# Optimization experiments

Hardware: AMD Instinct MI355X
Metric: run time of the kernel (lower is better)

Reference implementation:

```python
import jax, jax.numpy as jnp
import numpy as np

E = 64          # num experts
IN = 512        # input_size
OUT = 512       # output_size
N = 131072      # total tokens = sum(expert_size)
CAP = 3072      # static per-expert capacity (>= max expert_size)


def _make_expert_sizes():
    # uneven but deterministic sizes summing to N, all <= CAP
    rng = np.random.default_rng(0)
    sizes = np.full(E, N // E, dtype=np.int32)
    d = rng.integers(0, 513, size=E // 2).astype(np.int32)
    sizes[0::2] += d
    sizes[1::2] -= d
    assert sizes.sum() == N and sizes.max() <= CAP and sizes.min() > 0
    return jnp.asarray(sizes, dtype=jnp.int32)


def setup_inputs() -> dict:
    key = jax.random.key(0)
    k1, k2 = jax.random.split(key)
    inputs = jax.random.normal(k1, (N, IN), dtype=jnp.float32)
    # matches nn.init.uniform_(weight, -1/in, 1/in)
    weight = jax.random.uniform(k2, (E, IN, OUT), dtype=jnp.float32,
                                minval=-1.0 / IN, maxval=1.0 / IN)
    expert_size = _make_expert_sizes()
    return {"inputs": inputs, "expert_size": expert_size, "weight": weight}


def reference(inputs, expert_size, weight):
    # Grouped GEMM: tokens are pre-sorted by expert; segment e is
    # inputs[offset[e]:offset[e]+expert_size[e]] @ weight[e].
    cap_ids = jnp.arange(CAP, dtype=jnp.int32)                # [CAP]
    offsets = jnp.cumsum(expert_size) - expert_size           # [E]
    idx = offsets[:, None] + cap_ids[None, :]                 # [E, CAP]
    valid = cap_ids[None, :] < expert_size[:, None]           # [E, CAP]
    idx = jnp.where(valid, idx, N)                            # invalid -> OOB (dropped)
    # gather tokens into padded per-expert blocks; invalid slots -> 0
    x = jnp.take(inputs, idx, axis=0, mode='fill', fill_value=0.0)  # [E, CAP, IN]
    h = jnp.einsum('eci,eio->eco', x, weight)                 # [E, CAP, OUT]
    out = jnp.zeros((N, OUT), dtype=inputs.dtype)
    out = out.at[idx.reshape(-1)].add(h.reshape(-1, OUT), mode='drop')
    return out
```

## Files before the change

### kernel.cpp

```cpp
#include <hip/hip_runtime.h>
#include <hip/hip_bf16.h>

#define E_NUM 64
#define IN_SZ 512
#define OUT_SZ 512
#define N_TOK 131072
#define CAP 3072

#define BM 128
#define BN 256
#define BK 32
#define THREADS 256
#define RT_MAX 24
#define CT_NUM 2
#define JT 16

typedef __attribute__((ext_vector_type(8))) short short8;
typedef __attribute__((ext_vector_type(4))) float f32x4;

__device__ inline unsigned short f2bf(float f) {
    unsigned int u = __float_as_uint(f);
    unsigned int r = (u + 0x7FFF + ((u >> 16) & 1)) >> 16;
    return (unsigned short)r;
}

#define GLOAD_LDS16(g, l)                                                     \
    __builtin_amdgcn_global_load_lds(                                         \
        (const __attribute__((address_space(1))) void*)(g),                   \
        (__attribute__((address_space(3))) void*)(l), 16, 0, 0)

__global__ void offsets_kernel(const int* __restrict__ sizes, int* __restrict__ offs) {
    int e = threadIdx.x;
    int s = 0;
    for (int i = 0; i < e; ++i) s += sizes[i];
    offs[e] = s;
}

__global__ __launch_bounds__(256) void prep_wt(const float* __restrict__ W,
                                               unsigned short* __restrict__ WT) {
    __shared__ float t[32][33];
    int k0 = blockIdx.x * 32, n0 = blockIdx.y * 32, e = blockIdx.z;
    const float* We = W + (size_t)e * IN_SZ * OUT_SZ;
    int tid = threadIdx.x;
    int r = tid >> 3, c4 = (tid & 7) * 4;
    float4 v = *(const float4*)(We + (size_t)(k0 + r) * OUT_SZ + n0 + c4);
    t[r][c4 + 0] = v.x; t[r][c4 + 1] = v.y; t[r][c4 + 2] = v.z; t[r][c4 + 3] = v.w;
    __syncthreads();
    ushort4 o;
    o.x = f2bf(t[c4 + 0][r]);
    o.y = f2bf(t[c4 + 1][r]);
    o.z = f2bf(t[c4 + 2][r]);
    o.w = f2bf(t[c4 + 3][r]);
    unsigned short* O = WT + (size_t)e * IN_SZ * OUT_SZ + (size_t)(n0 + r) * IN_SZ + k0 + c4;
    *(ushort4*)O = o;
}

__global__ __launch_bounds__(THREADS, 2) void gemm_moe(
    const float* __restrict__ A, const int* __restrict__ sizes,
    const unsigned short* __restrict__ WT, const int* __restrict__ offs,
    float* __restrict__ out)
{
    int b0 = blockIdx.x;
    int wg = (b0 & 7) * (E_NUM * RT_MAX * CT_NUM / 8) + (b0 >> 3);
    int ct = wg & (CT_NUM - 1);
    int rt = (wg >> 1) % RT_MAX;
    int e  = wg / (RT_MAX * CT_NUM);

    int size_e = sizes[e];
    int rows0 = rt * BM;
    if (rows0 >= size_e) return;
    int off_e = offs[e];
    int rows_rem = size_e - rows0;
    int maxr = (rows_rem < BM ? rows_rem : BM) - 1;

    __shared__ unsigned short lsA[3][BM * BK];
    __shared__ unsigned short lsB[3][BN * BK];

    int tid = threadIdx.x, l = tid & 63, w = tid >> 6;
    const char* WTe = (const char*)(WT + (size_t)e * IN_SZ * OUT_SZ);
    const float* Abase = A + (size_t)(off_e + rows0) * IN_SZ;

    const float* ap[4];
    int aw[4];
    #pragma unroll
    for (int i = 0; i < 4; ++i) {
        int idx = tid + THREADS * i;
        int row = idx >> 3, c4 = idx & 7;
        int gr = row <= maxr ? row : maxr;
        ap[i] = Abase + (size_t)gr * IN_SZ + c4 * 4;
        aw[i] = row * 64 + ((c4 * 8) ^ (((row >> 1) & 3) << 4));
    }
    const char* gB[4];
    #pragma unroll
    for (int i = 0; i < 4; ++i) {
        int c = w * 4 + i;
        int n = c * 16 + (l >> 2);
        int csrc = ((l & 3) * 16) ^ (((l >> 3) & 3) << 4);
        gB[i] = WTe + (size_t)(ct * BN + n) * (IN_SZ * 2) + csrc;
    }

    float4 ar[2][4];

    auto loadA = [&](int kt, int p) {
        #pragma unroll
        for (int i = 0; i < 4; ++i)
            ar[p][i] = *(const float4*)(ap[i] + kt * BK);
    };
    auto writeA = [&](int buf, int p) {
        #pragma unroll
        for (int i = 0; i < 4; ++i) {
            ushort4 pk;
            pk.x = f2bf(ar[p][i].x); pk.y = f2bf(ar[p][i].y);
            pk.z = f2bf(ar[p][i].z); pk.w = f2bf(ar[p][i].w);
            *(ushort4*)((char*)&lsA[buf][0] + aw[i]) = pk;
        }
    };
    auto stageB = [&](int buf, int kt) {
        #pragma unroll
        for (int i = 0; i < 4; ++i)
            GLOAD_LDS16(gB[i] + kt * 64, &lsB[buf][(w * 4 + i) * 512]);
    };

    int wm = (w >> 1) * 64, wn = (w & 1) * 128;
    int lrow = l & 15;
    int cb = ((l >> 4) * 16) ^ (((l >> 1) & 3) << 4);

    f32x4 acc[4][8] = {};

    #define FRAGS_AND_MFMA(buf)                                               \
        {                                                                     \
            const char* pA = (const char*)&lsA[buf][0];                       \
            const char* pB = (const char*)&lsB[buf][0];                       \
            short8 af[4];                                                     \
            _Pragma("unroll")                                                 \
            for (int m = 0; m < 4; ++m)                                       \
                af[m] = *(const short8*)(pA + (wm + m * 16 + lrow) * 64 + cb);\
            short8 bfr[8];                                                    \
            _Pragma("unroll")                                                 \
            for (int n = 0; n < 8; ++n)                                       \
                bfr[n] = *(const short8*)(pB + (wn + n * 16 + lrow) * 64 + cb);\
            asm volatile("s_waitcnt lgkmcnt(0)" ::: "memory");                \
            __builtin_amdgcn_sched_barrier(0);                                \
            __builtin_amdgcn_s_setprio(1);                                    \
            _Pragma("unroll")                                                 \
            for (int m = 0; m < 4; ++m)                                       \
                _Pragma("unroll")                                             \
                for (int n = 0; n < 8; ++n)                                   \
                    acc[m][n] = __builtin_amdgcn_mfma_f32_16x16x32_bf16(      \
                        af[m], bfr[n], acc[m][n], 0, 0, 0);                   \
            __builtin_amdgcn_s_setprio(0);                                    \
        }

    loadA(0, 0); stageB(0, 0);
    loadA(1, 1); stageB(1, 1);
    writeA(0, 0);
    asm volatile("s_waitcnt vmcnt(8)" ::: "memory");
    __builtin_amdgcn_sched_barrier(0);
    asm volatile("s_waitcnt lgkmcnt(0)" ::: "memory");
    __builtin_amdgcn_sched_barrier(0);
    __builtin_amdgcn_s_barrier();
    __builtin_amdgcn_sched_barrier(0);

    #pragma unroll
    for (int j = 0; j < JT; ++j) {
        if (j + 2 < JT) {
            loadA(j + 2, (j + 2) & 1);
            stageB((j + 2) % 3, j + 2);
        }
        FRAGS_AND_MFMA(j % 3);
        if (j + 1 < JT)
            writeA((j + 1) % 3, (j + 1) & 1);
        if (j < JT - 1) {
            if (j < JT - 2) {
                asm volatile("s_waitcnt vmcnt(8)" ::: "memory");
            } else {
                asm volatile("s_waitcnt vmcnt(0)" ::: "memory");
            }
            __builtin_amdgcn_sched_barrier(0);
            asm volatile("s_waitcnt lgkmcnt(0)" ::: "memory");
            __builtin_amdgcn_sched_barrier(0);
            __builtin_amdgcn_s_barrier();
            __builtin_amdgcn_sched_barrier(0);
        }
    }

    float* outb = out + (size_t)(off_e + rows0) * OUT_SZ + ct * BN + wn;
    #pragma unroll
    for (int m = 0; m < 4; ++m) {
        #pragma unroll
        for (int j = 0; j < 4; ++j) {
            int rl = wm + m * 16 + (l >> 4) * 4 + j;
            if (rl < rows_rem) {
                float* po = outb + (size_t)rl * OUT_SZ + lrow;
                #pragma unroll
                for (int n = 0; n < 8; ++n)
                    po[n * 16] = acc[m][n][j];
            }
        }
    }
}

extern "C" void kernel_launch(void* const* d_in, const int* in_sizes, int n_in,
                              void* d_out, int out_size, void* d_ws, size_t ws_size,
                              hipStream_t stream) {
    const float* A      = (const float*)d_in[0];
    const int* sizes    = (const int*)d_in[1];
    const float* W      = (const float*)d_in[2];
    float* out          = (float*)d_out;

    unsigned short* WT  = (unsigned short*)d_ws;
    int* offs           = (int*)((char*)d_ws + (size_t)E_NUM * IN_SZ * OUT_SZ * 2);

    offsets_kernel<<<1, E_NUM, 0, stream>>>(sizes, offs);
    prep_wt<<<dim3(IN_SZ / 32, OUT_SZ / 32, E_NUM), 256, 0, stream>>>(W, WT);
    gemm_moe<<<E_NUM * RT_MAX * CT_NUM, THREADS, 0, stream>>>(A, sizes, WT, offs, out);
}
```

Measured before the change: 190.8 us.

## Stage fp32 A tiles directly to LDS and convert to bf16 at fragment load

The A operand is now staged with global_load_lds straight into shared memory as fp32, using an XOR swizzle. It is converted to bf16 with v_cvt_pk_bf16_f32 only after the fragments are read, instead of passing through registers and a manual rounding conversion before the LDS write. The B operand drops to double buffering while A keeps triple buffering, and the pipeline waits and barriers are restructured around this. The aim is to remove the register round-trip and VALU conversion work from the global-to-LDS path and to cut synchronisation. In exchange, A takes twice the LDS space and fragment-read bandwidth, and the conversion moves into the MFMA critical section.

```diff
diff --git a/kernel.cpp b/kernel.cpp
--- a/kernel.cpp
+++ b/kernel.cpp
@@ -17,11 +17,18 @@
 
 typedef __attribute__((ext_vector_type(8))) short short8;
 typedef __attribute__((ext_vector_type(4))) float f32x4;
+typedef __attribute__((ext_vector_type(4))) unsigned int u32x4;
 
 __device__ inline unsigned short f2bf(float f) {
     unsigned int u = __float_as_uint(f);
     unsigned int r = (u + 0x7FFF + ((u >> 16) & 1)) >> 16;
     return (unsigned short)r;
+}
+
+__device__ inline unsigned int cvtpk(float a, float b) {
+    unsigned int r;
+    asm("v_cvt_pk_bf16_f32 %0, %1, %2" : "=v"(r) : "v"(a), "v"(b));
+    return r;
 }
 
 #define GLOAD_LDS16(g, l)                                                     \
@@ -73,22 +80,19 @@
     int rows_rem = size_e - rows0;
     int maxr = (rows_rem < BM ? rows_rem : BM) - 1;
 
-    __shared__ unsigned short lsA[3][BM * BK];
-    __shared__ unsigned short lsB[3][BN * BK];
+    __shared__ float lsA[3][BM * BK];
+    __shared__ unsigned short lsB[2][BN * BK];
 
     int tid = threadIdx.x, l = tid & 63, w = tid >> 6;
     const char* WTe = (const char*)(WT + (size_t)e * IN_SZ * OUT_SZ);
-    const float* Abase = A + (size_t)(off_e + rows0) * IN_SZ;
-
-    const float* ap[4];
-    int aw[4];
+    const char* Abase = (const char*)(A + (size_t)(off_e + rows0) * IN_SZ);
+
+    const char* gA[4];
     #pragma unroll
     for (int i = 0; i < 4; ++i) {
-        int idx = tid + THREADS * i;
-        int row = idx >> 3, c4 = idx & 7;
+        int row = (w * 4 + i) * 8 + (l >> 3);
         int gr = row <= maxr ? row : maxr;
-        ap[i] = Abase + (size_t)gr * IN_SZ + c4 * 4;
-        aw[i] = row * 64 + ((c4 * 8) ^ (((row >> 1) & 3) << 4));
+        gA[i] = Abase + (size_t)gr * (IN_SZ * 4) + (((l & 7) ^ (row & 7)) * 16);
     }
     const char* gB[4];
     #pragma unroll
@@ -99,21 +103,10 @@
         gB[i] = WTe + (size_t)(ct * BN + n) * (IN_SZ * 2) + csrc;
     }
 
-    float4 ar[2][4];
-
-    auto loadA = [&](int kt, int p) {
+    auto stageA = [&](int buf, int kt) {
         #pragma unroll
         for (int i = 0; i < 4; ++i)
-            ar[p][i] = *(const float4*)(ap[i] + kt * BK);
-    };
-    auto writeA = [&](int buf, int p) {
-        #pragma unroll
-        for (int i = 0; i < 4; ++i) {
-            ushort4 pk;
-            pk.x = f2bf(ar[p][i].x); pk.y = f2bf(ar[p][i].y);
-            pk.z = f2bf(ar[p][i].z); pk.w = f2bf(ar[p][i].w);
-            *(ushort4*)((char*)&lsA[buf][0] + aw[i]) = pk;
-        }
+            GLOAD_LDS16(gA[i] + kt * 128, &lsA[buf][(w * 4 + i) * 256]);
     };
     auto stageB = [&](int buf, int kt) {
         #pragma unroll
@@ -122,25 +115,42 @@
     };
 
     int wm = (w >> 1) * 64, wn = (w & 1) * 128;
-    int lrow = l & 15;
-    int cb = ((l >> 4) * 16) ^ (((l >> 1) & 3) << 4);
+    int lrow = l & 15, kq = l >> 4;
+    int abm[4];
+    #pragma unroll
+    for (int m = 0; m < 4; ++m) abm[m] = (wm + m * 16 + lrow) * 128;
+    int as0 = ((kq * 2 + 0) ^ (lrow & 7)) * 16;
+    int as1 = ((kq * 2 + 1) ^ (lrow & 7)) * 16;
+    int cb = (kq * 16) ^ (((lrow >> 1) & 3) << 4);
 
     f32x4 acc[4][8] = {};
 
-    #define FRAGS_AND_MFMA(buf)                                               \
+    #define FRAGS_AND_MFMA(bufA, bufB)                                        \
         {                                                                     \
-            const char* pA = (const char*)&lsA[buf][0];                       \
-            const char* pB = (const char*)&lsB[buf][0];                       \
-            short8 af[4];                                                     \
-            _Pragma("unroll")                                                 \
-            for (int m = 0; m < 4; ++m)                                       \
-                af[m] = *(const short8*)(pA + (wm + m * 16 + lrow) * 64 + cb);\
+            const char* pA = (const char*)&lsA[bufA][0];                      \
+            const char* pB = (const char*)&lsB[bufB][0];                      \
+            f32x4 av[4][2];                                                   \
+            _Pragma("unroll")                                                 \
+            for (int m = 0; m < 4; ++m) {                                     \
+                av[m][0] = *(const f32x4*)(pA + abm[m] + as0);                \
+                av[m][1] = *(const f32x4*)(pA + abm[m] + as1);                \
+            }                                                                 \
             short8 bfr[8];                                                    \
             _Pragma("unroll")                                                 \
             for (int n = 0; n < 8; ++n)                                       \
                 bfr[n] = *(const short8*)(pB + (wn + n * 16 + lrow) * 64 + cb);\
             asm volatile("s_waitcnt lgkmcnt(0)" ::: "memory");                \
             __builtin_amdgcn_sched_barrier(0);                                \
+            short8 af[4];                                                     \
+            _Pragma("unroll")                                                 \
+            for (int m = 0; m < 4; ++m) {                                     \
+                u32x4 au;                                                     \
+                au[0] = cvtpk(av[m][0][0], av[m][0][1]);                      \
+                au[1] = cvtpk(av[m][0][2], av[m][0][3]);                      \
+                au[2] = cvtpk(av[m][1][0], av[m][1][1]);                      \
+                au[3] = cvtpk(av[m][1][2], av[m][1][3]);                      \
+                af[m] = __builtin_bit_cast(short8, au);                       \
+            }                                                                 \
             __builtin_amdgcn_s_setprio(1);                                    \
             _Pragma("unroll")                                                 \
             for (int m = 0; m < 4; ++m)                                       \
@@ -151,34 +161,25 @@
             __builtin_amdgcn_s_setprio(0);                                    \
         }
 
-    loadA(0, 0); stageB(0, 0);
-    loadA(1, 1); stageB(1, 1);
-    writeA(0, 0);
-    asm volatile("s_waitcnt vmcnt(8)" ::: "memory");
-    __builtin_amdgcn_sched_barrier(0);
-    asm volatile("s_waitcnt lgkmcnt(0)" ::: "memory");
+    stageA(0, 0); stageB(0, 0);
+    stageA(1, 1);
+    asm volatile("s_waitcnt vmcnt(4)" ::: "memory");
     __builtin_amdgcn_sched_barrier(0);
     __builtin_amdgcn_s_barrier();
     __builtin_amdgcn_sched_barrier(0);
 
     #pragma unroll
     for (int j = 0; j < JT; ++j) {
-        if (j + 2 < JT) {
-            loadA(j + 2, (j + 2) & 1);
-            stageB((j + 2) % 3, j + 2);
-        }
-        FRAGS_AND_MFMA(j % 3);
-        if (j + 1 < JT)
-            writeA((j + 1) % 3, (j + 1) & 1);
+        if (j + 1 < JT) stageB((j + 1) & 1, j + 1);
+        FRAGS_AND_MFMA(j % 3, j & 1);
+        if (j + 2 < JT) stageA((j + 2) % 3, j + 2);
         if (j < JT - 1) {
-            if (j < JT - 2) {
-                asm volatile("s_waitcnt vmcnt(8)" ::: "memory");
+            if (j + 2 < JT) {
+                asm volatile("s_waitcnt vmcnt(4)" ::: "memory");
             } else {
                 asm volatile("s_waitcnt vmcnt(0)" ::: "memory");
             }
             __builtin_amdgcn_sched_barrier(0);
-            asm volatile("s_waitcnt lgkmcnt(0)" ::: "memory");
-            __builtin_amdgcn_sched_barrier(0);
             __builtin_amdgcn_s_barrier();
             __builtin_amdgcn_sched_barrier(0);
         }
@@ -189,7 +190,7 @@
     for (int m = 0; m < 4; ++m) {
         #pragma unroll
         for (int j = 0; j < 4; ++j) {
-            int rl = wm + m * 16 + (l >> 4) * 4 + j;
+            int rl = wm + m * 16 + kq * 4 + j;
             if (rl < rows_rem) {
                 float* po = outb + (size_t)rl * OUT_SZ + lrow;
                 #pragma unroll
```

Result: faster. 187.0 us (median of 2 runs) (-2.0%).

## Shrink GEMM tile to 128x128 with double buffering for higher occupancy

Applied to the files above, without the earlier changes.

Halves the N tile from 256 to 128 and doubles the column tiles, so each block uses fewer accumulators and less LDS. The pipeline goes from three LDS stages to two, with a full vmcnt(0) wait every iteration, and launch bounds are raised to four blocks per CU. A fragments are now loaded inside the MFMA loop instead of all up front. The aim is more resident waves to hide latency, at the cost of A being re-read and converted twice as often (fp32 A is a major share of traffic) and a shallower prefetch.

```diff
diff --git a/kernel.cpp b/kernel.cpp
--- a/kernel.cpp
+++ b/kernel.cpp
@@ -8,12 +8,13 @@
 #define CAP 3072
 
 #define BM 128
-#define BN 256
+#define BN 128
 #define BK 32
 #define THREADS 256
 #define RT_MAX 24
-#define CT_NUM 2
+#define CT_NUM 4
 #define JT 16
+#define NWG (E_NUM * RT_MAX * CT_NUM)
 
 typedef __attribute__((ext_vector_type(8))) short short8;
 typedef __attribute__((ext_vector_type(4))) float f32x4;
@@ -55,15 +56,15 @@
     *(ushort4*)O = o;
 }
 
-__global__ __launch_bounds__(THREADS, 2) void gemm_moe(
+__global__ __launch_bounds__(THREADS, 4) void gemm_moe(
     const float* __restrict__ A, const int* __restrict__ sizes,
     const unsigned short* __restrict__ WT, const int* __restrict__ offs,
     float* __restrict__ out)
 {
     int b0 = blockIdx.x;
-    int wg = (b0 & 7) * (E_NUM * RT_MAX * CT_NUM / 8) + (b0 >> 3);
-    int ct = wg & (CT_NUM - 1);
-    int rt = (wg >> 1) % RT_MAX;
+    int wg = (b0 & 7) * (NWG / 8) + (b0 >> 3);
+    int ct = wg & 3;
+    int rt = (wg >> 2) % RT_MAX;
     int e  = wg / (RT_MAX * CT_NUM);
 
     int size_e = sizes[e];
@@ -73,8 +74,8 @@
     int rows_rem = size_e - rows0;
     int maxr = (rows_rem < BM ? rows_rem : BM) - 1;
 
-    __shared__ unsigned short lsA[3][BM * BK];
-    __shared__ unsigned short lsB[3][BN * BK];
+    __shared__ unsigned short lsA[2][BM * BK];
+    __shared__ unsigned short lsB[2][BN * BK];
 
     int tid = threadIdx.x, l = tid & 63, w = tid >> 6;
     const char* WTe = (const char*)(WT + (size_t)e * IN_SZ * OUT_SZ);
@@ -90,71 +91,66 @@
         ap[i] = Abase + (size_t)gr * IN_SZ + c4 * 4;
         aw[i] = row * 64 + ((c4 * 8) ^ (((row >> 1) & 3) << 4));
     }
-    const char* gB[4];
-    #pragma unroll
-    for (int i = 0; i < 4; ++i) {
-        int c = w * 4 + i;
+    const char* gB[2];
+    #pragma unroll
+    for (int i = 0; i < 2; ++i) {
+        int c = w * 2 + i;
         int n = c * 16 + (l >> 2);
         int csrc = ((l & 3) * 16) ^ (((l >> 3) & 3) << 4);
         gB[i] = WTe + (size_t)(ct * BN + n) * (IN_SZ * 2) + csrc;
     }
 
-    float4 ar[2][4];
-
-    auto loadA = [&](int kt, int p) {
+    float4 ar[4];
+
+    auto loadA = [&](int kt) {
         #pragma unroll
         for (int i = 0; i < 4; ++i)
-            ar[p][i] = *(const float4*)(ap[i] + kt * BK);
+            ar[i] = *(const float4*)(ap[i] + kt * BK);
     };
-    auto writeA = [&](int buf, int p) {
+    auto writeA = [&](int buf) {
         #pragma unroll
         for (int i = 0; i < 4; ++i) {
             ushort4 pk;
-            pk.x = f2bf(ar[p][i].x); pk.y = f2bf(ar[p][i].y);
-            pk.z = f2bf(ar[p][i].z); pk.w = f2bf(ar[p][i].w);
+            pk.x = f2bf(ar[i].x); pk.y = f2bf(ar[i].y);
+            pk.z = f2bf(ar[i].z); pk.w = f2bf(ar[i].w);
             *(ushort4*)((char*)&lsA[buf][0] + aw[i]) = pk;
         }
     };
     auto stageB = [&](int buf, int kt) {
         #pragma unroll
-        for (int i = 0; i < 4; ++i)
-            GLOAD_LDS16(gB[i] + kt * 64, &lsB[buf][(w * 4 + i) * 512]);
+        for (int i = 0; i < 2; ++i)
+            GLOAD_LDS16(gB[i] + kt * 64, &lsB[buf][(w * 2 + i) * 512]);
     };
 
-    int wm = (w >> 1) * 64, wn = (w & 1) * 128;
+    int wm = (w >> 1) * 64, wn = (w & 1) * 64;
     int lrow = l & 15;
     int cb = ((l >> 4) * 16) ^ (((l >> 1) & 3) << 4);
 
-    f32x4 acc[4][8] = {};
+    f32x4 acc[4][4] = {};
 
     #define FRAGS_AND_MFMA(buf)                                               \
         {                                                                     \
             const char* pA = (const char*)&lsA[buf][0];                       \
             const char* pB = (const char*)&lsB[buf][0];                       \
-            short8 af[4];                                                     \
+            short8 bfr[4];                                                    \
             _Pragma("unroll")                                                 \
-            for (int m = 0; m < 4; ++m)                                       \
-                af[m] = *(const short8*)(pA + (wm + m * 16 + lrow) * 64 + cb);\
-            short8 bfr[8];                                                    \
-            _Pragma("unroll")                                                 \
-            for (int n = 0; n < 8; ++n)                                       \
+            for (int n = 0; n < 4; ++n)                                       \
                 bfr[n] = *(const short8*)(pB + (wn + n * 16 + lrow) * 64 + cb);\
-            asm volatile("s_waitcnt lgkmcnt(0)" ::: "memory");                \
-            __builtin_amdgcn_sched_barrier(0);                                \
             __builtin_amdgcn_s_setprio(1);                                    \
             _Pragma("unroll")                                                 \
-            for (int m = 0; m < 4; ++m)                                       \
+            for (int m = 0; m < 4; ++m) {                                     \
+                short8 af = *(const short8*)(pA + (wm + m * 16 + lrow) * 64 + cb);\
                 _Pragma("unroll")                                             \
-                for (int n = 0; n < 8; ++n)                                   \
+                for (int n = 0; n < 4; ++n)                                   \
                     acc[m][n] = __builtin_amdgcn_mfma_f32_16x16x32_bf16(      \
-                        af[m], bfr[n], acc[m][n], 0, 0, 0);                   \
+                        af, bfr[n], acc[m][n], 0, 0, 0);                      \
+            }                                                                 \
             __builtin_amdgcn_s_setprio(0);                                    \
         }
 
-    loadA(0, 0); stageB(0, 0);
-    loadA(1, 1); stageB(1, 1);
-    writeA(0, 0);
-    asm volatile("s_waitcnt vmcnt(8)" ::: "memory");
+    loadA(0); stageB(0, 0);
+    writeA(0);
+    asm volatile("s_waitcnt vmcnt(0)" ::: "memory");
     __builtin_amdgcn_sched_barrier(0);
     asm volatile("s_waitcnt lgkmcnt(0)" ::: "memory");
     __builtin_amdgcn_sched_barrier(0);
@@ -163,19 +159,16 @@
 
     #pragma unroll
     for (int j = 0; j < JT; ++j) {
-        if (j + 2 < JT) {
-            loadA(j + 2, (j + 2) & 1);
-            stageB((j + 2) % 3, j + 2);
-        }
-        FRAGS_AND_MFMA(j % 3);
+        int cur = j & 1;
+        if (j + 1 < JT) {
+            loadA(j + 1);
+            stageB(cur ^ 1, j + 1);
+        }
+        FRAGS_AND_MFMA(cur);
         if (j + 1 < JT)
-            writeA((j + 1) % 3, (j + 1) & 1);
+            writeA(cur ^ 1);
         if (j < JT - 1) {
-            if (j < JT - 2) {
-                asm volatile("s_waitcnt vmcnt(8)" ::: "memory");
-            } else {
-                asm volatile("s_waitcnt vmcnt(0)" ::: "memory");
-            }
+            asm volatile("s_waitcnt vmcnt(0)" ::: "memory");
             __builtin_amdgcn_sched_barrier(0);
             asm volatile("s_waitcnt lgkmcnt(0)" ::: "memory");
             __builtin_amdgcn_sched_barrier(0);
@@ -193,7 +186,7 @@
             if (rl < rows_rem) {
                 float* po = outb + (size_t)rl * OUT_SZ + lrow;
                 #pragma unroll
-                for (int n = 0; n < 8; ++n)
+                for (int n = 0; n < 4; ++n)
                     po[n * 16] = acc[m][n][j];
             }
         }
@@ -213,5 +206,5 @@
 
     offsets_kernel<<<1, E_NUM, 0, stream>>>(sizes, offs);
     prep_wt<<<dim3(IN_SZ / 32, OUT_SZ / 32, E_NUM), 256, 0, stream>>>(W, WT);
-    gemm_moe<<<E_NUM * RT_MAX * CT_NUM, THREADS, 0, stream>>>(A, sizes, WT, offs, out);
-}
+    gemm_moe<<<NWG, THREADS, 0, stream>>>(A, sizes, WT, offs, out);
+}
```

After: 245.1 us. +28.5%, slower.
